# Optimization experiments

Hardware: AMD Instinct MI355X
Metric: run time of the kernel (lower is better)

The kernel has to match this reference:

```python
import jax, jax.numpy as jnp
import numpy as np

N = 4096          # total nodes
G = 8             # graphs in batch
M_PER = N // G    # nodes per graph (contiguous batch ids)
DEG = 8           # random out-edges per node before symmetrization (~16 after)


def setup_inputs() -> dict:
    rng = np.random.default_rng(0)
    A = np.zeros((N, N), dtype=np.float32)
    for g in range(G):
        lo = g * M_PER
        u = rng.integers(lo, lo + M_PER, size=M_PER * DEG)
        v = rng.integers(lo, lo + M_PER, size=M_PER * DEG)
        A[u, v] = 1.0
        ring = np.arange(lo, lo + M_PER)           # guarantee no isolated nodes
        A[ring, np.roll(ring, -1)] = 1.0
    A = np.maximum(A, A.T)                          # undirected (symmetric)
    np.fill_diagonal(A, 0.0)                        # no self loops
    batch = np.repeat(np.arange(G), M_PER).astype(np.int64)
    return {"A": jnp.asarray(A), "batch": jnp.asarray(batch), "num_graphs": G}


def _netsimile_node_features(A):
    # Vectorized form of the per-node ego-network loop.
    # Row n of M1 is the boolean mask of the 1-hop egonet {n} U N(n);
    # B = M1 @ A counts, for each (n, v), edges from ego1(n) into v, so
    # M2 = M1 | (B > 0) is the 2-hop egonet mask. All loop statistics become
    # row reductions of these matrices.
    n = A.shape[0]
    deg = A.sum(axis=1)                                  # [N] feat0: degree
    deg_safe = jnp.maximum(deg, 1.0)
    f0 = deg
    f2 = jnp.where(deg > 0, (A @ deg) / deg_safe, 0.0)   # scatter_mean(deg[col], row)

    eye = jnp.eye(n, dtype=A.dtype)
    M1 = jnp.maximum(A, eye)                             # [N,N] 1-hop ego masks
    B = M1 @ A                                           # [N,N] one-step reach counts
    f4_raw = (B * M1).sum(axis=1)                        # directed edges inside ego1
    M2 = jnp.maximum(M1, (B > 0).astype(A.dtype))        # [N,N] 2-hop ego masks
    f5 = M2 @ deg - 2.0 * f4_raw                         # sum(mask2[row]) - 2*feat4 (incl. post-loop -=)
    f6 = M2.sum(axis=1) - deg - 1.0                      # |ego2| - deg - 1

    denom = jnp.where(deg > 1, deg * (deg - 1.0), 1.0)
    f1 = jnp.where(deg > 1, (f4_raw - deg) / denom, 0.0)  # clustering coeff
    # undirected graph corrections (data.is_undirected() is True)
    f1 = f1 * 2.0
    f4 = f4_raw / 2.0
    f3 = jnp.where(deg > 0, (A @ f1) / deg_safe, 0.0)     # scatter_mean(f1[col], row)
    return jnp.stack([f0, f1, f2, f3, f4, f5, f6], axis=1)  # [N,7]


def reference(A, batch, num_graphs):
    feat = _netsimile_node_features(A)                   # [N,7]
    n, F = feat.shape
    m = n // num_graphs                                  # equal-size contiguous graphs
    xg = feat.reshape(num_graphs, m, F)                  # batch ids are sorted blocks
    mean = xg.mean(axis=1)                               # [G,7]
    c = xg - mean[:, None, :]
    m2 = (c ** 2).mean(axis=1)
    m3 = (c ** 3).mean(axis=1)
    m4 = (c ** 4).mean(axis=1)
    # torch.median returns the LOWER middle element for even counts
    median = jnp.sort(xg, axis=1)[:, (m - 1) // 2, :]
    eps = jnp.float32(1e-4)
    skew = m3 / jnp.maximum(m2 ** 1.5, eps)
    kurt = m4 / jnp.maximum(m2 ** 2, eps)
    return jnp.hstack([mean, median, jnp.sqrt(m2), skew, kurt])  # [G,35]
```

## Files before the change

### kernel.cpp

```cpp
#include <hip/hip_runtime.h>
#include <stdint.h>

typedef unsigned long long u64;

#define NNODE 4096
#define NG    8
#define M     512
#define W     8

#define OFF_MASK 0
#define OFF_DEG  (262144)
#define OFF_F1   (262144 + 16384)
#define OFF_FEAT (262144 + 32768)

__global__ __launch_bounds__(256) void k_pack(const float* __restrict__ A,
                                              u64* __restrict__ gmask,
                                              float* __restrict__ gdeg) {
    int row  = (blockIdx.x << 2) + (threadIdx.x >> 6);
    int lane = threadIdx.x & 63;
    int lo   = (row >> 9) << 9;
    const float* rowp = A + (size_t)row * NNODE + lo;
    float4 a = *(const float4*)(rowp + lane * 8);
    float4 b = *(const float4*)(rowp + lane * 8 + 4);
    unsigned int byte =
        (a.x != 0.f ? 1u : 0u) | (a.y != 0.f ? 2u : 0u) |
        (a.z != 0.f ? 4u : 0u) | (a.w != 0.f ? 8u : 0u) |
        (b.x != 0.f ? 16u : 0u) | (b.y != 0.f ? 32u : 0u) |
        (b.z != 0.f ? 64u : 0u) | (b.w != 0.f ? 128u : 0u);
    ((unsigned char*)gmask)[(size_t)row * 64 + lane] = (unsigned char)byte;
    int c = __popc(byte);
#pragma unroll
    for (int off = 32; off; off >>= 1) c += __shfl_down(c, off, 64);
    if (lane == 0) gdeg[row] = (float)c;
}

static __device__ __forceinline__ u64 shfl_xor_u64(u64 v, int mask) {
    return ((u64)(unsigned)__shfl_xor((int)(v >> 32), mask, 64) << 32) |
           (u64)(unsigned)__shfl_xor((int)(v & 0xffffffffu), mask, 64);
}

__global__ __launch_bounds__(256) void k_feat(const u64* __restrict__ gmask,
                                              const float* __restrict__ gdeg,
                                              float* __restrict__ featg,
                                              float* __restrict__ f1g) {
    int g = blockIdx.x >> 3, chunk = blockIdx.x & 7;
    int t = threadIdx.x;
    __shared__ u64 smT[W * M];
    __shared__ float sdeg[M];
    __shared__ u64 planes[9][W];

    const u64* gm = gmask + (size_t)g * M * W;
    for (int idx = t; idx < M * W; idx += 256) {
        int u = idx >> 3, w = idx & 7;
        smT[w * M + u] = gm[idx];
    }
    for (int i = t; i < M; i += 256) sdeg[i] = gdeg[g * M + i];
    __syncthreads();

    int wv = t >> 6, lane = t & 63;
    for (int w = wv; w < W; w += 4) {
        int d = (int)sdeg[(w << 6) + lane];
#pragma unroll
        for (int k = 0; k < 9; k++) {
            u64 bal = __ballot(((d >> k) & 1) != 0);
            if (lane == 0) planes[k][w] = bal;
        }
    }
    __syncthreads();

    int nl = t >> 2, q = t & 3;
    int n  = chunk * 64 + nl;
    u64 m1[W], reach[W];
#pragma unroll
    for (int w = 0; w < W; w++) { m1[w] = smT[w * M + n]; reach[w] = 0ull; }
    m1[n >> 6] |= 1ull << (n & 63);

    int f4 = 0;
#pragma unroll
    for (int wq = 0; wq < 2; wq++) {
        int w = 2 * q + wq;
        u64 bits = m1[w];
        while (bits) {
            int b = __ffsll(bits) - 1;
            bits &= bits - 1;
            int u = (w << 6) + b;
#pragma unroll
            for (int w2 = 0; w2 < W; w2++) {
                u64 r = smT[w2 * M + u];
                reach[w2] |= r;
                f4 += __popcll(r & m1[w2]);
            }
        }
    }
    f4 += __shfl_xor(f4, 1, 64);
    f4 += __shfl_xor(f4, 2, 64);
#pragma unroll
    for (int w = 0; w < W; w++) {
        reach[w] |= shfl_xor_u64(reach[w], 1);
        reach[w] |= shfl_xor_u64(reach[w], 2);
    }

    if (q == 0) {
        int f6c = 0;
        u64 m2m[W];
#pragma unroll
        for (int w = 0; w < W; w++) { m2m[w] = m1[w] | reach[w]; f6c += __popcll(m2m[w]); }
        int f5i = 0, f2i = 0;
        u64 arow_self = 1ull << (n & 63);
#pragma unroll
        for (int k = 0; k < 9; k++) {
            int c5 = 0, c2 = 0;
#pragma unroll
            for (int w = 0; w < W; w++) {
                u64 ar = (w == (n >> 6)) ? (m1[w] & ~arow_self) : m1[w];
                c5 += __popcll(m2m[w] & planes[k][w]);
                c2 += __popcll(ar & planes[k][w]);
            }
            f5i += c5 << k;
            f2i += c2 << k;
        }
        float deg = sdeg[n];
        float f4raw = (float)f4;
        float f1 = (deg > 1.f) ? 2.f * (f4raw - deg) / (deg * (deg - 1.f)) : 0.f;
        float* fb = featg + (size_t)g * 7 * M;
        fb[0 * M + n] = deg;
        fb[1 * M + n] = f1;
        fb[2 * M + n] = (deg > 0.f) ? (float)f2i / deg : 0.f;
        fb[4 * M + n] = f4raw * 0.5f;
        fb[5 * M + n] = (float)f5i - 2.f * f4raw;
        fb[6 * M + n] = (float)f6c - deg - 1.f;
        f1g[g * M + n] = f1;
    }
}

__global__ __launch_bounds__(512) void k_f3(const u64* __restrict__ gmask,
                                            const float* __restrict__ gdeg,
                                            const float* __restrict__ f1g,
                                            float* __restrict__ featg) {
    int g = blockIdx.x;
    int t = threadIdx.x;
    __shared__ float f1s[M];
    f1s[t] = f1g[g * M + t];
    __syncthreads();

    const u64* m = gmask + ((size_t)g * M + t) * W;
    float sum = 0.f;
#pragma unroll
    for (int w = 0; w < W; w++) {
        u64 bits = m[w];
        while (bits) {
            int b = __ffsll(bits) - 1;
            bits &= bits - 1;
            sum += f1s[(w << 6) + b];
        }
    }
    float deg = gdeg[g * M + t];
    featg[(size_t)g * 7 * M + 3 * M + t] = (deg > 0.f) ? sum / deg : 0.f;
}

__global__ __launch_bounds__(256) void k_stats(const float* __restrict__ featg,
                                               float* __restrict__ out) {
    int blk = blockIdx.x;
    int gf = blk >> 1, half = blk & 1;
    int g = gf / 7, f = gf % 7;
    int t = threadIdx.x;
    __shared__ __align__(16) float sv[M];
    __shared__ double rsum[4], r2[4], r3[4], r4[4];
    __shared__ double smean;

    sv[t]       = featg[(size_t)gf * M + t];
    sv[t + 256] = featg[(size_t)gf * M + t + 256];
    __syncthreads();

    int wv = t >> 6, lane = t & 63;
    if (half == 0) {
        double s = (double)sv[t] + (double)sv[t + 256];
#pragma unroll
        for (int off = 32; off; off >>= 1) s += __shfl_xor(s, off, 64);
        if (lane == 0) rsum[wv] = s;
        __syncthreads();
        if (t == 0) smean = (rsum[0] + rsum[1] + rsum[2] + rsum[3]) * (1.0 / 512.0);
        __syncthreads();
        double mean = smean;
        double c1 = (double)sv[t] - mean, c2v = (double)sv[t + 256] - mean;
        double a2 = c1 * c1, b2 = c2v * c2v;
        double p2 = a2 + b2, p3 = a2 * c1 + b2 * c2v, p4 = a2 * a2 + b2 * b2;
#pragma unroll
        for (int off = 32; off; off >>= 1) {
            p2 += __shfl_xor(p2, off, 64);
            p3 += __shfl_xor(p3, off, 64);
            p4 += __shfl_xor(p4, off, 64);
        }
        if (lane == 0) { r2[wv] = p2; r3[wv] = p3; r4[wv] = p4; }
        __syncthreads();
        if (t == 0) {
            double m2 = (r2[0] + r2[1] + r2[2] + r2[3]) * (1.0 / 512.0);
            double m3 = (r3[0] + r3[1] + r3[2] + r3[3]) * (1.0 / 512.0);
            double m4 = (r4[0] + r4[1] + r4[2] + r4[3]) * (1.0 / 512.0);
            double sd = sqrt(m2);
            double den3 = m2 * sd;  if (den3 < 1e-4) den3 = 1e-4;
            double den4 = m2 * m2;  if (den4 < 1e-4) den4 = 1e-4;
            out[g * 35 + f]      = (float)smean;
            out[g * 35 + 14 + f] = (float)sd;
            out[g * 35 + 21 + f] = (float)(m3 / den3);
            out[g * 35 + 28 + f] = (float)(m4 / den4);
        }
    }

    float cv = sv[half * 256 + t];
    int less = 0, eq = 0;
    for (int j = 0; j < M; j += 4) {
        float4 x = *(const float4*)&sv[j];
        less += (x.x < cv) + (x.y < cv) + (x.z < cv) + (x.w < cv);
        eq   += (x.x == cv) + (x.y == cv) + (x.z == cv) + (x.w == cv);
    }
    if (less <= 255 && less + eq > 255) out[g * 35 + 7 + f] = cv;
}

extern "C" void kernel_launch(void* const* d_in, const int* in_sizes, int n_in,
                              void* d_out, int out_size, void* d_ws, size_t ws_size,
                              hipStream_t stream) {
    const float* A = (const float*)d_in[0];
    float* out = (float*)d_out;
    char* ws = (char*)d_ws;
    u64*   gmask = (u64*)(ws + OFF_MASK);
    float* gdeg  = (float*)(ws + OFF_DEG);
    float* f1g   = (float*)(ws + OFF_F1);
    float* featg = (float*)(ws + OFF_FEAT);

    k_pack <<<NNODE / 4, 256, 0, stream>>>(A, gmask, gdeg);
    k_feat <<<NG * 8,    256, 0, stream>>>(gmask, gdeg, featg, f1g);
    k_f3   <<<NG,        512, 0, stream>>>(gmask, gdeg, f1g, featg);
    k_stats<<<NG * 7 * 2, 256, 0, stream>>>(featg, out);
}
```

Baseline: 114.8 us.

## Spread ego-net feature work across 16 lanes per node and more blocks

k_feat now uses 16 threads per node instead of 4, each walking a 32-bit slice of the 1-hop mask. The per-word reach masks are combined with a butterfly shuffle reduction, and the plane popcounts for f2/f5/f6 are split across lanes and summed by shuffles. The grid grows from 64 to 256 blocks, and the shared-memory fill uses 128-bit loads. k_f3 is also split into 64 blocks of 64 threads. The aim is to fill more CUs and shorten the serial bit-iteration per thread, at the cost of more blocks each reloading the graph's mask into LDS and more shuffle traffic.

```diff
diff --git a/kernel.cpp b/kernel.cpp
--- a/kernel.cpp
+++ b/kernel.cpp
@@ -43,16 +43,20 @@
                                               const float* __restrict__ gdeg,
                                               float* __restrict__ featg,
                                               float* __restrict__ f1g) {
-    int g = blockIdx.x >> 3, chunk = blockIdx.x & 7;
+    int g = blockIdx.x >> 5, chunk = blockIdx.x & 31;
     int t = threadIdx.x;
     __shared__ u64 smT[W * M];
     __shared__ float sdeg[M];
     __shared__ u64 planes[9][W];
 
-    const u64* gm = gmask + (size_t)g * M * W;
-    for (int idx = t; idx < M * W; idx += 256) {
-        int u = idx >> 3, w = idx & 7;
-        smT[w * M + u] = gm[idx];
+    const ulonglong2* gm2 = (const ulonglong2*)(gmask + (size_t)g * M * W);
+#pragma unroll
+    for (int it = 0; it < 8; it++) {
+        int idx = t + (it << 8);
+        ulonglong2 v = gm2[idx];
+        int u = idx >> 2, w2 = (idx & 3) << 1;
+        smT[w2 * M + u]       = v.x;
+        smT[(w2 + 1) * M + u] = v.y;
     }
     for (int i = t; i < M; i += 256) sdeg[i] = gdeg[g * M + i];
     __syncthreads();
@@ -68,64 +72,95 @@
     }
     __syncthreads();
 
-    int nl = t >> 2, q = t & 3;
-    int n  = chunk * 64 + nl;
-    u64 m1[W], reach[W];
-#pragma unroll
-    for (int w = 0; w < W; w++) { m1[w] = smT[w * M + n]; reach[w] = 0ull; }
+    int nl = t >> 4, q = t & 15;
+    int n  = (chunk << 4) + nl;
+
+    u64 m1[W];
+#pragma unroll
+    for (int ww = 0; ww < W; ww++) m1[ww] = smT[ww * M + n];
     m1[n >> 6] |= 1ull << (n & 63);
 
+    u64 reach[W];
+#pragma unroll
+    for (int ww = 0; ww < W; ww++) reach[ww] = 0ull;
+
+    int w = q >> 1, h = q & 1;
+    u64 myw = smT[w * M + n];
+    if (w == (n >> 6)) myw |= 1ull << (n & 63);
+    unsigned int bits = h ? (unsigned int)(myw >> 32) : (unsigned int)myw;
+    int base = (w << 6) + (h << 5);
+
     int f4 = 0;
-#pragma unroll
-    for (int wq = 0; wq < 2; wq++) {
-        int w = 2 * q + wq;
-        u64 bits = m1[w];
-        while (bits) {
-            int b = __ffsll(bits) - 1;
-            bits &= bits - 1;
-            int u = (w << 6) + b;
-#pragma unroll
-            for (int w2 = 0; w2 < W; w2++) {
-                u64 r = smT[w2 * M + u];
-                reach[w2] |= r;
-                f4 += __popcll(r & m1[w2]);
-            }
-        }
-    }
-    f4 += __shfl_xor(f4, 1, 64);
-    f4 += __shfl_xor(f4, 2, 64);
-#pragma unroll
-    for (int w = 0; w < W; w++) {
-        reach[w] |= shfl_xor_u64(reach[w], 1);
-        reach[w] |= shfl_xor_u64(reach[w], 2);
+    while (bits) {
+        int b = __ffs(bits) - 1;
+        bits &= bits - 1;
+        int u = base + b;
+#pragma unroll
+        for (int w2 = 0; w2 < W; w2++) {
+            u64 r = smT[w2 * M + u];
+            reach[w2] |= r;
+            f4 += __popcll(r & m1[w2]);
+        }
+    }
+
+    u64 s4[4];
+#pragma unroll
+    for (int i = 0; i < 4; i++) {
+        u64 keep = (q & 1) ? reach[i + 4] : reach[i];
+        u64 send = (q & 1) ? reach[i]     : reach[i + 4];
+        s4[i] = keep | shfl_xor_u64(send, 1);
+    }
+    u64 s2[2];
+#pragma unroll
+    for (int i = 0; i < 2; i++) {
+        u64 keep = (q & 2) ? s4[i + 2] : s4[i];
+        u64 send = (q & 2) ? s4[i]     : s4[i + 2];
+        s2[i] = keep | shfl_xor_u64(send, 2);
+    }
+    u64 s1;
+    {
+        u64 keep = (q & 4) ? s2[1] : s2[0];
+        u64 send = (q & 4) ? s2[0] : s2[1];
+        s1 = keep | shfl_xor_u64(send, 4);
+    }
+    u64 rfin = s1 | shfl_xor_u64(s1, 8);
+    int wq = ((q & 1) << 2) | (q & 2) | ((q >> 2) & 1);
+
+    u64 aw  = smT[wq * M + n];
+    u64 m1w = aw;
+    if (wq == (n >> 6)) m1w |= 1ull << (n & 63);
+    u64 m2m = m1w | rfin;
+
+    int f5f6 = 0, f2p = 0;
+    if (q < 8) {
+        int acc = __popcll(m2m) << 20;
+#pragma unroll
+        for (int k = 0; k < 9; k++) acc += __popcll(m2m & planes[k][wq]) << k;
+        f5f6 = acc;
+    } else {
+        int acc = 0;
+#pragma unroll
+        for (int k = 0; k < 9; k++) acc += __popcll(aw & planes[k][wq]) << k;
+        f2p = acc;
+    }
+
+#pragma unroll
+    for (int mk = 1; mk <= 8; mk <<= 1) {
+        f4   += __shfl_xor(f4,   mk, 64);
+        f5f6 += __shfl_xor(f5f6, mk, 64);
+        f2p  += __shfl_xor(f2p,  mk, 64);
     }
 
     if (q == 0) {
-        int f6c = 0;
-        u64 m2m[W];
-#pragma unroll
-        for (int w = 0; w < W; w++) { m2m[w] = m1[w] | reach[w]; f6c += __popcll(m2m[w]); }
-        int f5i = 0, f2i = 0;
-        u64 arow_self = 1ull << (n & 63);
-#pragma unroll
-        for (int k = 0; k < 9; k++) {
-            int c5 = 0, c2 = 0;
-#pragma unroll
-            for (int w = 0; w < W; w++) {
-                u64 ar = (w == (n >> 6)) ? (m1[w] & ~arow_self) : m1[w];
-                c5 += __popcll(m2m[w] & planes[k][w]);
-                c2 += __popcll(ar & planes[k][w]);
-            }
-            f5i += c5 << k;
-            f2i += c2 << k;
-        }
+        int f5i = f5f6 & 0xFFFFF;
+        int f6c = f5f6 >> 20;
         float deg = sdeg[n];
         float f4raw = (float)f4;
         float f1 = (deg > 1.f) ? 2.f * (f4raw - deg) / (deg * (deg - 1.f)) : 0.f;
         float* fb = featg + (size_t)g * 7 * M;
         fb[0 * M + n] = deg;
         fb[1 * M + n] = f1;
-        fb[2 * M + n] = (deg > 0.f) ? (float)f2i / deg : 0.f;
+        fb[2 * M + n] = (deg > 0.f) ? (float)f2p / deg : 0.f;
         fb[4 * M + n] = f4raw * 0.5f;
         fb[5 * M + n] = (float)f5i - 2.f * f4raw;
         fb[6 * M + n] = (float)f6c - deg - 1.f;
@@ -133,29 +168,31 @@
     }
 }
 
-__global__ __launch_bounds__(512) void k_f3(const u64* __restrict__ gmask,
-                                            const float* __restrict__ gdeg,
-                                            const float* __restrict__ f1g,
-                                            float* __restrict__ featg) {
-    int g = blockIdx.x;
+__global__ __launch_bounds__(64) void k_f3(const u64* __restrict__ gmask,
+                                           const float* __restrict__ gdeg,
+                                           const float* __restrict__ f1g,
+                                           float* __restrict__ featg) {
+    int g = blockIdx.x >> 3, chunk = blockIdx.x & 7;
     int t = threadIdx.x;
     __shared__ float f1s[M];
-    f1s[t] = f1g[g * M + t];
-    __syncthreads();
-
-    const u64* m = gmask + ((size_t)g * M + t) * W;
+#pragma unroll
+    for (int i = 0; i < 8; i++) f1s[t + (i << 6)] = f1g[g * M + t + (i << 6)];
+    __syncthreads();
+
+    int n = (chunk << 6) + t;
+    const u64* mrow = gmask + ((size_t)g * M + n) * W;
     float sum = 0.f;
 #pragma unroll
     for (int w = 0; w < W; w++) {
-        u64 bits = m[w];
+        u64 bits = mrow[w];
         while (bits) {
             int b = __ffsll(bits) - 1;
             bits &= bits - 1;
             sum += f1s[(w << 6) + b];
         }
     }
-    float deg = gdeg[g * M + t];
-    featg[(size_t)g * 7 * M + 3 * M + t] = (deg > 0.f) ? sum / deg : 0.f;
+    float deg = gdeg[g * M + n];
+    featg[(size_t)g * 7 * M + 3 * M + n] = (deg > 0.f) ? sum / deg : 0.f;
 }
 
 __global__ __launch_bounds__(256) void k_stats(const float* __restrict__ featg,
@@ -229,7 +266,7 @@
     float* featg = (float*)(ws + OFF_FEAT);
 
     k_pack <<<NNODE / 4, 256, 0, stream>>>(A, gmask, gdeg);
-    k_feat <<<NG * 8,    256, 0, stream>>>(gmask, gdeg, featg, f1g);
-    k_f3   <<<NG,        512, 0, stream>>>(gmask, gdeg, f1g, featg);
+    k_feat <<<NG * 32,   256, 0, stream>>>(gmask, gdeg, featg, f1g);
+    k_f3   <<<NG * 8,     64, 0, stream>>>(gmask, gdeg, f1g, featg);
     k_stats<<<NG * 7 * 2, 256, 0, stream>>>(featg, out);
 }
```

Measured after the change: 108.9 us. 1.06x faster.
